# Kernel tuning notes

Hardware: AMD Instinct MI355X
Metric: run time of the kernel (lower is better)

Reference implementation:

```python
import jax, jax.numpy as jnp
import numpy as np

EMBED_DIM = 1024
NUM_HEADS = 16
HEAD_DIM = EMBED_DIM // NUM_HEADS
SEQ_LEN = 2048
BATCH = 2
THETA_BASE = 10000.0


def rope_angles(head_dim, max_seq_len):
    inv_freq = 1.0 / (THETA_BASE ** (jnp.arange(0, head_dim, 2, dtype=jnp.float32) / head_dim))
    pos = jnp.arange(max_seq_len, dtype=jnp.float32)
    angles = pos[:, None] * inv_freq[None, :]              # [S, D/2]
    angles = jnp.concatenate([angles, angles], axis=-1)    # [S, D]
    return jnp.cos(angles), jnp.sin(angles)


def apply_rope(x, cos, sin):
    # x: [B, H, S, D]; cos/sin: [S, D]
    d = x.shape[-1]
    x1, x2 = x[..., : d // 2], x[..., d // 2 :]
    rotated = jnp.concatenate([-x2, x1], axis=-1)
    return x * cos[None, None, :, :] + rotated * sin[None, None, :, :]


def setup_inputs() -> dict:
    key = jax.random.key(0)
    kx, kq, kk, kv, ko = jax.random.split(key, 5)
    s = 1.0 / np.sqrt(EMBED_DIM)
    return {
        "x": jax.random.normal(kx, (BATCH, SEQ_LEN, EMBED_DIM), dtype=jnp.float32),
        "Wq": jax.random.normal(kq, (EMBED_DIM, EMBED_DIM), dtype=jnp.float32) * s,
        "Wk": jax.random.normal(kk, (EMBED_DIM, EMBED_DIM), dtype=jnp.float32) * s,
        "Wv": jax.random.normal(kv, (EMBED_DIM, EMBED_DIM), dtype=jnp.float32) * s,
        "Wo": jax.random.normal(ko, (EMBED_DIM, EMBED_DIM), dtype=jnp.float32) * s,
    }


def reference(x, Wq, Wk, Wv, Wo):
    B, S, E = x.shape
    H, D = NUM_HEADS, HEAD_DIM
    cos, sin = rope_angles(D, S)

    def split_heads(t):
        return t.reshape(B, S, H, D).transpose(0, 2, 1, 3)  # [B,H,S,D]

    q = split_heads(x @ Wq.T)
    k = split_heads(x @ Wk.T)
    v = split_heads(x @ Wv.T)

    q = apply_rope(q, cos, sin)
    k = apply_rope(k, cos, sin)

    scores = jnp.einsum("bhsd,bhtd->bhst", q, k)
    causal = jnp.triu(jnp.ones((S, S), dtype=bool), k=1)
    scores = jnp.where(causal[None, None, :, :], -jnp.inf, scores)
    weights = jax.nn.softmax(scores / jnp.sqrt(jnp.float32(D)), axis=-1)

    ctx = jnp.einsum("bhst,bhtd->bhsd", weights, v)
    ctx = ctx.transpose(0, 2, 1, 3).reshape(B, S, E)
    return ctx @ Wo.T
```

## Files before the change

### kernel.cpp

```cpp
#include <hip/hip_runtime.h>
#include <hip/hip_bf16.h>

#define H_NUM 16
#define D_DIM 64
#define S_LEN 2048
#define EMB   1024
#define M_TOT 4096

typedef unsigned short u16;
typedef unsigned int   u32;
typedef __attribute__((ext_vector_type(8))) short short8;
typedef __attribute__((ext_vector_type(4))) float f32x4;

__device__ __forceinline__ u32 f2bf_u(float f) {
    u32 u = __float_as_uint(f);
    return (u + 0x7fffu + ((u >> 16) & 1u)) >> 16;
}
__device__ __forceinline__ u32 pack2(float a, float b) {
    return f2bf_u(a) | (f2bf_u(b) << 16);
}
__device__ __forceinline__ uint4 pack8(float4 lo, float4 hi) {
    return make_uint4(pack2(lo.x, lo.y), pack2(lo.z, lo.w),
                      pack2(hi.x, hi.y), pack2(hi.z, hi.w));
}

__device__ __forceinline__ void lds_dma16(const u16* g, u16* l) {
    __builtin_amdgcn_global_load_lds(
        (const __attribute__((address_space(1))) void*)g,
        (__attribute__((address_space(3))) void*)l, 16, 0, 0);
}

__global__ __launch_bounds__(256) void cast_kernel(
    const float* __restrict__ x,  const float* __restrict__ Wq,
    const float* __restrict__ Wk, const float* __restrict__ Wv,
    const float* __restrict__ Wo, u16* __restrict__ ws, float2* __restrict__ tab)
{
    const int seg = blockIdx.y;
    if (seg == 5) {
        const int idx = blockIdx.x * 256 + threadIdx.x;
        if (idx < S_LEN * 32) {
            const int s = idx >> 5, d = idx & 31;
            const float ang = (float)s * __expf(-(float)d * 0.28782313662425573f);
            tab[idx] = make_float2(cosf(ang), sinf(ang));
        }
        return;
    }
    const float* src = (seg == 0) ? x : (seg == 1) ? Wq : (seg == 2) ? Wk
                     : (seg == 3) ? Wv : Wo;
    u16* dst = (seg == 0) ? ws : ws + (3 + seg) * 1048576;
    const int n = (seg == 0) ? 4194304 : 1048576;
    const int idx = (blockIdx.x * 256 + threadIdx.x) * 8;
    if (idx < n) {
        float4 lo = *(const float4*)(src + idx);
        float4 hi = *(const float4*)(src + idx + 4);
        *(uint4*)(dst + idx) = pack8(lo, hi);
    }
}

__global__ __launch_bounds__(256) void qkv_rope_kernel(
    const u16* __restrict__ xb, const u16* __restrict__ wb,
    const float2* __restrict__ tab,
    u16* __restrict__ qo, u16* __restrict__ ko, u16* __restrict__ vo)
{
    const int w  = blockIdx.y >> 3;
    const int nb = blockIdx.y & 7;
    const u16* W = wb + w * 1048576;

    __shared__ __align__(16) u16 smem[12288];
    u16* As = smem;
    u16* Bs = smem + 64 * 64;
    u16 (*Ep)[132] = (u16(*)[132])smem;

    const int tid   = threadIdx.x;
    const int lane  = tid & 63;
    const int wid   = tid >> 6;
    const int waveM = wid >> 1;
    const int waveN = wid & 1;
    const int col16 = lane & 15;
    const int quad  = lane >> 4;

    const int m0 = blockIdx.x * 64;
    const int n0 = nb * 128;

    f32x4 acc[2][4];
    const f32x4 zero4 = {0.f, 0.f, 0.f, 0.f};
#pragma unroll
    for (int i = 0; i < 2; i++)
#pragma unroll
        for (int j = 0; j < 4; j++) acc[i][j] = zero4;

    const int drow = tid >> 3;
    const int dpos = tid & 7;
    const u16* Ag = xb + (size_t)m0 * EMB;
    const u16* Bg = W  + (size_t)n0 * EMB;

    for (int k0 = 0; k0 < EMB; k0 += 64) {
        __syncthreads();
#pragma unroll
        for (int j = 0; j < 2; j++) {
            const int rl = j * 32 + drow;
            const int cg = dpos ^ (rl & 7);
            lds_dma16(Ag + (size_t)rl * EMB + k0 + cg * 8,
                      As + (j * 32 + wid * 8) * 64);
        }
#pragma unroll
        for (int j = 0; j < 4; j++) {
            const int rl = j * 32 + drow;
            const int cg = dpos ^ (rl & 7);
            lds_dma16(Bg + (size_t)rl * EMB + k0 + cg * 8,
                      Bs + (j * 32 + wid * 8) * 64);
        }
        __syncthreads();

        short8 af[2][2], bf[4][2];
#pragma unroll
        for (int mt = 0; mt < 2; mt++) {
            const int r = waveM * 32 + mt * 16 + col16;
#pragma unroll
            for (int ks = 0; ks < 2; ks++) {
                const int p = (ks * 4 + quad) ^ (r & 7);
                af[mt][ks] = *(const short8*)(As + r * 64 + p * 8);
            }
        }
#pragma unroll
        for (int nt = 0; nt < 4; nt++) {
            const int r = waveN * 64 + nt * 16 + col16;
#pragma unroll
            for (int ks = 0; ks < 2; ks++) {
                const int p = (ks * 4 + quad) ^ (r & 7);
                bf[nt][ks] = *(const short8*)(Bs + r * 64 + p * 8);
            }
        }
#pragma unroll
        for (int ks = 0; ks < 2; ks++)
#pragma unroll
            for (int mt = 0; mt < 2; mt++)
#pragma unroll
                for (int nt = 0; nt < 4; nt++)
                    acc[mt][nt] = __builtin_amdgcn_mfma_f32_16x16x32_bf16(
                        af[mt][ks], bf[nt][ks], acc[mt][nt], 0, 0, 0);
    }

    __syncthreads();
#pragma unroll
    for (int mt = 0; mt < 2; mt++) {
#pragma unroll
        for (int r = 0; r < 4; r++) {
            const int m_local = waveM * 32 + mt * 16 + quad * 4 + r;
            const int s = (m0 + m_local) & 2047;
            if (w == 2) {
#pragma unroll
                for (int nt = 0; nt < 4; nt++)
                    Ep[m_local][waveN * 64 + nt * 16 + col16] =
                        (u16)f2bf_u(acc[mt][nt][r]);
            } else {
#pragma unroll
                for (int nt = 0; nt < 2; nt++) {
                    const int d = nt * 16 + col16;
                    const float2 cs = tab[s * 32 + d];
                    const float lo = acc[mt][nt][r];
                    const float hi = acc[mt][nt + 2][r];
                    Ep[m_local][waveN * 64 + d]      = (u16)f2bf_u(lo * cs.x - hi * cs.y);
                    Ep[m_local][waveN * 64 + d + 32] = (u16)f2bf_u(hi * cs.x + lo * cs.y);
                }
            }
        }
    }
    __syncthreads();

    const int b = m0 >> 11;
    if (w != 2) {
        u16* out = (w == 0) ? qo : ko;
#pragma unroll
        for (int j = 0; j < 4; j++) {
            const int g = j * 256 + tid;
            const int head_local = g >> 9;
            const int sl  = (g >> 3) & 63;
            const int cir = g & 7;
            uint4 val = *(const uint4*)(&Ep[sl][head_local * 64 + cir * 8]);
            const int h = (n0 >> 6) + head_local;
            const size_t base = (((size_t)(b * H_NUM + h)) * S_LEN + (m0 & 2047)) * 64;
            *(uint4*)(out + base + (size_t)(g & 511) * 8) = val;
        }
    } else {
        const int s0 = m0 & 2047;
#pragma unroll
        for (int j = 0; j < 4; j++) {
            const int g = j * 256 + tid;
            const int d_all = g >> 3;
            const int sc = g & 7;
            u32 wv[4];
#pragma unroll
            for (int hw = 0; hw < 4; hw++) {
                const int p0 = sc * 8 + hw * 2;
                const int r0 = ((p0 & 3) << 4) | (p0 >> 2);
                const int p1 = p0 + 1;
                const int r1 = ((p1 & 3) << 4) | (p1 >> 2);
                wv[hw] = (u32)Ep[r0][d_all] | ((u32)Ep[r1][d_all] << 16);
            }
            const int h = (n0 >> 6) + (d_all >> 6);
            const int d = d_all & 63;
            *(uint4*)(vo + ((size_t)(b * H_NUM + h) * 64 + d) * 2048 + s0 + sc * 8) =
                make_uint4(wv[0], wv[1], wv[2], wv[3]);
        }
    }
}

__global__ __launch_bounds__(256) void attn_kernel(
    const u16* __restrict__ q, const u16* __restrict__ k,
    const u16* __restrict__ v, u16* __restrict__ ctx)
{
    __shared__ __align__(16) u16 QP[64 * 64];
    __shared__ __align__(16) u16 Ks[64 * 64];
    __shared__ __align__(16) u16 VTs[64 * 64];

    const int tid   = threadIdx.x;
    const int lane  = tid & 63;
    const int wid   = tid >> 6;
    const int col16 = lane & 15;
    const int quad  = lane >> 4;

    const int bh    = blockIdx.x;
    const int qb    = 31 - blockIdx.y;
    const int qBase = qb * 64;
    const size_t bhOff = (size_t)bh * S_LEN * D_DIM;

    const int drow = tid >> 3;
    const int dpos = tid & 7;

#pragma unroll
    for (int j = 0; j < 2; j++) {
        const int rl = j * 32 + drow;
        const int cg = dpos ^ (rl & 7);
        lds_dma16(q + bhOff + (size_t)(qBase + rl) * 64 + cg * 8,
                  QP + (j * 32 + wid * 8) * 64);
    }
    __syncthreads();

    short8 qf[2];
    {
        const int rq = wid * 16 + col16;
#pragma unroll
        for (int ks = 0; ks < 2; ks++) {
            const int c = (ks * 4 + quad) ^ (rq & 7);
            qf[ks] = *(const short8*)(QP + rq * 64 + c * 8);
        }
    }

    f32x4 O[4];
    const f32x4 zero4 = {0.f, 0.f, 0.f, 0.f};
#pragma unroll
    for (int j = 0; j < 4; j++) O[j] = zero4;
    float lrun[4] = {0.f, 0.f, 0.f, 0.f};

    const float K2 = 0.18033688011112042f;

    for (int kt = 0; kt <= qb; kt++) {
        __syncthreads();
#pragma unroll
        for (int j = 0; j < 2; j++) {
            const int rl = j * 32 + drow;
            const int cg = dpos ^ (rl & 7);
            lds_dma16(k + bhOff + (size_t)(kt * 64 + rl) * 64 + cg * 8,
                      Ks + (j * 32 + wid * 8) * 64);
        }
#pragma unroll
        for (int j = 0; j < 2; j++) {
            const int rl = j * 32 + drow;
            const int cg = dpos ^ (rl & 7);
            lds_dma16(v + bhOff + (size_t)rl * 2048 + kt * 64 + cg * 8,
                      VTs + (j * 32 + wid * 8) * 64);
        }
        __syncthreads();

        f32x4 sc[4];
#pragma unroll
        for (int nt = 0; nt < 4; nt++) sc[nt] = zero4;
#pragma unroll
        for (int ks = 0; ks < 2; ks++) {
            short8 kf[4];
#pragma unroll
            for (int nt = 0; nt < 4; nt++) {
                const int rk = nt * 16 + col16;
                const int c = (ks * 4 + quad) ^ (rk & 7);
                kf[nt] = *(const short8*)(Ks + rk * 64 + c * 8);
            }
#pragma unroll
            for (int nt = 0; nt < 4; nt++)
                sc[nt] = __builtin_amdgcn_mfma_f32_16x16x32_bf16(
                    qf[ks], kf[nt], sc[nt], 0, 0, 0);
        }

        if (kt == qb) {
#pragma unroll
            for (int r = 0; r < 4; r++) {
                const int qg = qBase + wid * 16 + quad * 4 + r;
                float lsum = 0.f;
#pragma unroll
                for (int nt = 0; nt < 4; nt++) {
                    const int kg = kt * 64 + nt * 16 + col16;
                    float sv = fmaf(sc[nt][r], K2, -16.0f);
                    if (kg > qg) sv = -INFINITY;
                    const float p = exp2f(sv);
                    sc[nt][r] = p;
                    lsum += p;
                }
                lrun[r] += lsum;
            }
        } else {
#pragma unroll
            for (int r = 0; r < 4; r++) {
                float lsum = 0.f;
#pragma unroll
                for (int nt = 0; nt < 4; nt++) {
                    const float p = exp2f(fmaf(sc[nt][r], K2, -16.0f));
                    sc[nt][r] = p;
                    lsum += p;
                }
                lrun[r] += lsum;
            }
        }

#pragma unroll
        for (int r = 0; r < 4; r++) {
            const int ml = quad * 4 + r;
            const u32 lo = pack2(sc[0][r], sc[1][r]);
            const u32 hi = pack2(sc[2][r], sc[3][r]);
            *(uint2*)(QP + (wid * 16 + ml) * 64 +
                      (((col16 >> 1) ^ (ml & 7)) * 8 + (col16 & 1) * 4)) =
                make_uint2(lo, hi);
        }

#pragma unroll
        for (int ks = 0; ks < 2; ks++) {
            short8 pf, vf[4];
            {
                const int c = (ks * 4 + quad) ^ (col16 & 7);
                pf = *(const short8*)(QP + (wid * 16 + col16) * 64 + c * 8);
            }
#pragma unroll
            for (int dt = 0; dt < 4; dt++) {
                const int d = dt * 16 + col16;
                const int c = (ks * 4 + quad) ^ (d & 7);
                vf[dt] = *(const short8*)(VTs + d * 64 + c * 8);
            }
#pragma unroll
            for (int dt = 0; dt < 4; dt++)
                O[dt] = __builtin_amdgcn_mfma_f32_16x16x32_bf16(
                    pf, vf[dt], O[dt], 0, 0, 0);
        }
    }

#pragma unroll
    for (int r = 0; r < 4; r++) {
#pragma unroll
        for (int o = 1; o < 16; o <<= 1)
            lrun[r] += __shfl_xor(lrun[r], o);
    }

    const int b = bh >> 4, h = bh & 15;
#pragma unroll
    for (int r = 0; r < 4; r++) {
        const int ml = quad * 4 + r;
        const float inv = 1.0f / lrun[r];
        const u32 lo = pack2(O[0][r] * inv, O[1][r] * inv);
        const u32 hi = pack2(O[2][r] * inv, O[3][r] * inv);
        *(uint2*)(QP + (wid * 16 + ml) * 64 +
                  (((col16 >> 1) ^ (ml & 7)) * 8 + (col16 & 1) * 4)) =
            make_uint2(lo, hi);
    }
#pragma unroll
    for (int j = 0; j < 2; j++) {
        const int g  = j * 64 + lane;
        const int sl = g >> 3;
        const int cir = g & 7;
        u32 wv[4];
#pragma unroll
        for (int hw = 0; hw < 4; hw++) {
            const int d0 = cir * 8 + hw * 2;
            const int p0 = ((d0 & 15) << 2) | (d0 >> 4);
            const int d1 = d0 + 1;
            const int p1 = ((d1 & 15) << 2) | (d1 >> 4);
            const u16 v0 = QP[(wid * 16 + sl) * 64 + ((p0 >> 3) ^ (sl & 7)) * 8 + (p0 & 7)];
            const u16 v1 = QP[(wid * 16 + sl) * 64 + ((p1 >> 3) ^ (sl & 7)) * 8 + (p1 & 7)];
            wv[hw] = (u32)v0 | ((u32)v1 << 16);
        }
        const size_t rowbase =
            ((size_t)b * S_LEN + qBase + wid * 16 + sl) * EMB + h * 64;
        *(uint4*)(ctx + rowbase + cir * 8) = make_uint4(wv[0], wv[1], wv[2], wv[3]);
    }
}

__global__ __launch_bounds__(256) void proj_kernel(
    const u16* __restrict__ X, const u16* __restrict__ W, float* __restrict__ out)
{
    __shared__ __align__(16) u16 smem[12288];
    u16* As = smem;
    u16* Bs = smem + 64 * 64;

    const int tid   = threadIdx.x;
    const int lane  = tid & 63;
    const int wid   = tid >> 6;
    const int waveM = wid >> 1;
    const int waveN = wid & 1;
    const int col16 = lane & 15;
    const int quad  = lane >> 4;

    const int m0 = blockIdx.x * 64;
    const int n0 = blockIdx.y * 128;

    f32x4 acc[4][2];
    const f32x4 zero4 = {0.f, 0.f, 0.f, 0.f};
#pragma unroll
    for (int i = 0; i < 4; i++)
#pragma unroll
        for (int j = 0; j < 2; j++) acc[i][j] = zero4;

    const int drow = tid >> 3;
    const int dpos = tid & 7;
    const u16* Ag = X + (size_t)m0 * EMB;
    const u16* Bg = W + (size_t)n0 * EMB;

    for (int k0 = 0; k0 < EMB; k0 += 64) {
        __syncthreads();
#pragma unroll
        for (int j = 0; j < 2; j++) {
            const int rl = j * 32 + drow;
            const int cg = dpos ^ (rl & 7);
            lds_dma16(Ag + (size_t)rl * EMB + k0 + cg * 8,
                      As + (j * 32 + wid * 8) * 64);
        }
#pragma unroll
        for (int j = 0; j < 4; j++) {
            const int rl = j * 32 + drow;
            const int cg = dpos ^ (rl & 7);
            lds_dma16(Bg + (size_t)rl * EMB + k0 + cg * 8,
                      Bs + (j * 32 + wid * 8) * 64);
        }
        __syncthreads();

        short8 af[2][2], bf[4][2];
#pragma unroll
        for (int mt = 0; mt < 2; mt++) {
            const int r = waveM * 32 + mt * 16 + col16;
#pragma unroll
            for (int ks = 0; ks < 2; ks++) {
                const int p = (ks * 4 + quad) ^ (r & 7);
                af[mt][ks] = *(const short8*)(As + r * 64 + p * 8);
            }
        }
#pragma unroll
        for (int nt = 0; nt < 4; nt++) {
            const int r = waveN * 64 + nt * 16 + col16;
#pragma unroll
            for (int ks = 0; ks < 2; ks++) {
                const int p = (ks * 4 + quad) ^ (r & 7);
                bf[nt][ks] = *(const short8*)(Bs + r * 64 + p * 8);
            }
        }
#pragma unroll
        for (int ks = 0; ks < 2; ks++)
#pragma unroll
            for (int nt = 0; nt < 4; nt++)
#pragma unroll
                for (int mt = 0; mt < 2; mt++)
                    acc[nt][mt] = __builtin_amdgcn_mfma_f32_16x16x32_bf16(
                        bf[nt][ks], af[mt][ks], acc[nt][mt], 0, 0, 0);
    }

#pragma unroll
    for (int nt = 0; nt < 4; nt++)
#pragma unroll
        for (int mt = 0; mt < 2; mt++) {
            const int m_g = m0 + waveM * 32 + mt * 16 + col16;
            const int n_g = n0 + waveN * 64 + nt * 16 + quad * 4;
            *(f32x4*)(out + (size_t)m_g * EMB + n_g) = acc[nt][mt];
        }
}

extern "C" void kernel_launch(void* const* d_in, const int* in_sizes, int n_in,
                              void* d_out, int out_size, void* d_ws, size_t ws_size,
                              hipStream_t stream)
{
    const float* x  = (const float*)d_in[0];
    const float* Wq = (const float*)d_in[1];
    const float* Wk = (const float*)d_in[2];
    const float* Wv = (const float*)d_in[3];
    const float* Wo = (const float*)d_in[4];

    u16* ws = (u16*)d_ws;
    u16* xb  = ws;
    u16* wb  = ws + 4194304;
    u16* wob = ws + 7340032;
    u16* q   = ws + 8388608;
    u16* k   = ws + 12582912;
    u16* v   = ws + 16777216;
    u16* ctx = ws + 20971520;
    float2* tab = (float2*)(ws + 25165824);

    cast_kernel<<<dim3(2048, 6), 256, 0, stream>>>(x, Wq, Wk, Wv, Wo, ws, tab);
    qkv_rope_kernel<<<dim3(64, 24), 256, 0, stream>>>(xb, wb, tab, q, k, v);
    attn_kernel<<<dim3(32, 32), 256, 0, stream>>>(q, k, v, ctx);
    proj_kernel<<<dim3(64, 8), 256, 0, stream>>>(ctx, wob, (float*)d_out);
}
```

Before: 178.8 us.

## Halve attention query tile to 32 rows and pack bf16 by truncation

```diff
diff --git a/kernel.cpp b/kernel.cpp
--- a/kernel.cpp
+++ b/kernel.cpp
@@ -18,6 +18,10 @@
 }
 __device__ __forceinline__ u32 pack2(float a, float b) {
     return f2bf_u(a) | (f2bf_u(b) << 16);
+}
+__device__ __forceinline__ u32 pack2t(float a, float b) {
+    return __builtin_amdgcn_perm(__float_as_uint(b), __float_as_uint(a),
+                                 0x07060302u);
 }
 __device__ __forceinline__ uint4 pack8(float4 lo, float4 hi) {
     return make_uint4(pack2(lo.x, lo.y), pack2(lo.z, lo.w),
@@ -206,11 +210,11 @@
     }
 }
 
-__global__ __launch_bounds__(256) void attn_kernel(
+__global__ __launch_bounds__(128) void attn_kernel(
     const u16* __restrict__ q, const u16* __restrict__ k,
     const u16* __restrict__ v, u16* __restrict__ ctx)
 {
-    __shared__ __align__(16) u16 QP[64 * 64];
+    __shared__ __align__(16) u16 QP[32 * 64];
     __shared__ __align__(16) u16 Ks[64 * 64];
     __shared__ __align__(16) u16 VTs[64 * 64];
 
@@ -221,19 +225,19 @@
     const int quad  = lane >> 4;
 
     const int bh    = blockIdx.x;
-    const int qb    = 31 - blockIdx.y;
-    const int qBase = qb * 64;
+    const int qb    = 63 - blockIdx.y;
+    const int qBase = qb * 32;
     const size_t bhOff = (size_t)bh * S_LEN * D_DIM;
 
-    const int drow = tid >> 3;
-    const int dpos = tid & 7;
+    const int lrow8 = lane >> 3;
+    const int lpos  = lane & 7;
 
 #pragma unroll
     for (int j = 0; j < 2; j++) {
-        const int rl = j * 32 + drow;
-        const int cg = dpos ^ (rl & 7);
+        const int rl = j * 16 + wid * 8 + lrow8;
+        const int cg = lpos ^ (rl & 7);
         lds_dma16(q + bhOff + (size_t)(qBase + rl) * 64 + cg * 8,
-                  QP + (j * 32 + wid * 8) * 64);
+                  QP + (j * 16 + wid * 8) * 64);
     }
     __syncthreads();
 
@@ -254,22 +258,23 @@
     float lrun[4] = {0.f, 0.f, 0.f, 0.f};
 
     const float K2 = 0.18033688011112042f;
-
-    for (int kt = 0; kt <= qb; kt++) {
+    const int ktEnd = (qBase + 31) >> 6;
+
+    for (int kt = 0; kt <= ktEnd; kt++) {
         __syncthreads();
 #pragma unroll
-        for (int j = 0; j < 2; j++) {
-            const int rl = j * 32 + drow;
-            const int cg = dpos ^ (rl & 7);
+        for (int j = 0; j < 4; j++) {
+            const int rl = j * 16 + wid * 8 + lrow8;
+            const int cg = lpos ^ (rl & 7);
             lds_dma16(k + bhOff + (size_t)(kt * 64 + rl) * 64 + cg * 8,
-                      Ks + (j * 32 + wid * 8) * 64);
-        }
-#pragma unroll
-        for (int j = 0; j < 2; j++) {
-            const int rl = j * 32 + drow;
-            const int cg = dpos ^ (rl & 7);
+                      Ks + (j * 16 + wid * 8) * 64);
+        }
+#pragma unroll
+        for (int j = 0; j < 4; j++) {
+            const int rl = j * 16 + wid * 8 + lrow8;
+            const int cg = lpos ^ (rl & 7);
             lds_dma16(v + bhOff + (size_t)rl * 2048 + kt * 64 + cg * 8,
-                      VTs + (j * 32 + wid * 8) * 64);
+                      VTs + (j * 16 + wid * 8) * 64);
         }
         __syncthreads();
 
@@ -291,7 +296,7 @@
                     qf[ks], kf[nt], sc[nt], 0, 0, 0);
         }
 
-        if (kt == qb) {
+        if (kt == ktEnd) {
 #pragma unroll
             for (int r = 0; r < 4; r++) {
                 const int qg = qBase + wid * 16 + quad * 4 + r;
@@ -324,8 +329,8 @@
 #pragma unroll
         for (int r = 0; r < 4; r++) {
             const int ml = quad * 4 + r;
-            const u32 lo = pack2(sc[0][r], sc[1][r]);
-            const u32 hi = pack2(sc[2][r], sc[3][r]);
+            const u32 lo = pack2t(sc[0][r], sc[1][r]);
+            const u32 hi = pack2t(sc[2][r], sc[3][r]);
             *(uint2*)(QP + (wid * 16 + ml) * 64 +
                       (((col16 >> 1) ^ (ml & 7)) * 8 + (col16 & 1) * 4)) =
                 make_uint2(lo, hi);
@@ -363,8 +368,8 @@
     for (int r = 0; r < 4; r++) {
         const int ml = quad * 4 + r;
         const float inv = 1.0f / lrun[r];
-        const u32 lo = pack2(O[0][r] * inv, O[1][r] * inv);
-        const u32 hi = pack2(O[2][r] * inv, O[3][r] * inv);
+        const u32 lo = pack2t(O[0][r] * inv, O[1][r] * inv);
+        const u32 hi = pack2t(O[2][r] * inv, O[3][r] * inv);
         *(uint2*)(QP + (wid * 16 + ml) * 64 +
                   (((col16 >> 1) ^ (ml & 7)) * 8 + (col16 & 1) * 4)) =
             make_uint2(lo, hi);
@@ -500,6 +505,6 @@
 
     cast_kernel<<<dim3(2048, 6), 256, 0, stream>>>(x, Wq, Wk, Wv, Wo, ws, tab);
     qkv_rope_kernel<<<dim3(64, 24), 256, 0, stream>>>(xb, wb, tab, q, k, v);
-    attn_kernel<<<dim3(32, 32), 256, 0, stream>>>(q, k, v, ctx);
+    attn_kernel<<<dim3(32, 64), 128, 0, stream>>>(q, k, v, ctx);
     proj_kernel<<<dim3(64, 8), 256, 0, stream>>>(ctx, wob, (float*)d_out);
 }
```

New measurement: 183.2 us. 1.03x slower.
